# Kernel optimization log

Measured on AMD Instinct MI355X. Metric: run time of the kernel, lower is better.

The kernel has to match this reference:

```python
import jax, jax.numpy as jnp
import numpy as np

DENSITY = 985.0  # kg/m^3, body density used by BodyMeasurements for mass
EPS = 1e-12


def _measure(v_shaped, faces_tensor, circ_vert_idx, height_vert_idx):
    # Gather triangles: [B, F, 3(verts), 3(xyz)]
    tris = v_shaped[:, faces_tensor]
    v0, v1, v2 = tris[:, :, 0, :], tris[:, :, 1, :], tris[:, :, 2, :]

    # --- mass: signed tetrahedron volumes summed over faces ---
    vol = jnp.einsum('bfi,bfi->b', v0, jnp.cross(v1, v2)) / 6.0
    mass = jnp.abs(vol) * DENSITY                       # [B]

    # --- height: vertical distance between two landmark vertices ---
    height = jnp.abs(v_shaped[:, height_vert_idx[0], 1]
                     - v_shaped[:, height_vert_idx[1], 1])  # [B]

    # --- circumferences: horizontal plane y = y(landmark) intersected with mesh ---
    plane_y = v_shaped[:, circ_vert_idx, 1]             # [B, M] per-batch plane heights
    pa = tris                                           # edge starts  [B,F,3,3]
    pb = jnp.roll(tris, -1, axis=2)                     # edge ends    [B,F,3,3]
    ya = pa[..., 1]                                     # [B,F,3]
    yb = pb[..., 1]
    py = plane_y[:, None, None, :]                      # [B,1,1,M]
    da = ya[..., None] - py                             # signed dist of edge start [B,F,3,M]
    db = yb[..., None] - py
    crossing = (da * db) < 0.0                          # edge straddles plane
    t = da / jnp.where(crossing, da - db, 1.0)          # safe param along edge
    # intersection points on the plane: [B,F,3(edges),M,3]
    pts = pa[..., None, :] + t[..., None] * (pb - pa)[..., None, :]
    # a crossing triangle has exactly 2 crossing edges -> one active edge pair
    pts_n = jnp.roll(pts, -1, axis=2)
    pair_ok = crossing & jnp.roll(crossing, -1, axis=2)  # [B,F,3,M]
    d = jnp.where(pair_ok[..., None], pts_n - pts, 0.0)
    seg_len = jnp.sqrt(jnp.sum(d * d, axis=-1) + EPS) * pair_ok  # [B,F,3,M]
    circ = jnp.sum(seg_len, axis=(1, 2))                # [B, M]

    # mass, height, chest, waist, hips -> [B, 5]
    return jnp.concatenate([mass[:, None], height[:, None], circ], axis=1)


def setup_inputs() -> dict:
    key = jax.random.key(0)
    k1, k2, k3, k4 = jax.random.split(key, 4)
    B, V, F = 256, 6890, 13776
    v_shaped = jax.random.normal(k1, (B, V, 3), dtype=jnp.float32)
    faces_tensor = jax.random.randint(k2, (F, 3), 0, V)
    circ_vert_idx = jax.random.randint(k3, (3,), 0, V)
    height_vert_idx = jax.random.randint(k4, (2,), 0, V)
    return {
        'v_shaped': v_shaped,
        'faces_tensor': faces_tensor,
        'circ_vert_idx': circ_vert_idx,
        'height_vert_idx': height_vert_idx,
    }


def reference(v_shaped, faces_tensor, circ_vert_idx, height_vert_idx):
    return _measure(v_shaped, faces_tensor, circ_vert_idx, height_vert_idx)
```

## Files before the change

### kernel.cpp

```cpp
#include <hip/hip_runtime.h>
#include <math.h>

#define NV      6890
#define BLOCK   1024
#define NWAVES  (BLOCK / 64)
#define DENSITY 985.0f
#define EPS     1e-12f

typedef float v2f __attribute__((ext_vector_type(2)));

__device__ __forceinline__ float frcp(float x)  { return __builtin_amdgcn_rcpf(x); }
__device__ __forceinline__ float fsqrt(float x) { return __builtin_amdgcn_sqrtf(x); }

__global__ __launch_bounds__(BLOCK) void measure_kernel(
    const float* __restrict__ v,
    const int*   __restrict__ faces,
    const int*   __restrict__ circ_idx,
    const int*   __restrict__ h_idx,
    float*       __restrict__ out,
    int F)
{
    extern __shared__ float lds[];
    v2f*   xzs = reinterpret_cast<v2f*>(lds);
    float* ys  = lds + 2 * NV;
    float* red = ys + NV;

    const int b = blockIdx.x;
    const float* vb = v + (size_t)b * NV * 3;

    for (int i = threadIdx.x; i < NV; i += BLOCK) {
        const float* p = vb + 3 * i;
        const float x = p[0], y = p[1], z = p[2];
        ys[i] = y;
        xzs[i] = (v2f){ x, z };
    }
    __syncthreads();

    const float pys[3] = { ys[circ_idx[0]], ys[circ_idx[1]], ys[circ_idx[2]] };

    float vol = 0.0f;
    float circ[3] = {0.0f, 0.0f, 0.0f};

    #pragma unroll 2
    for (int f = threadIdx.x; f < F; f += BLOCK) {
        const int i0 = faces[3 * f + 0];
        const int i1 = faces[3 * f + 1];
        const int i2 = faces[3 * f + 2];

        const float y0 = ys[i0], y1 = ys[i1], y2 = ys[i2];
        const v2f xz0 = xzs[i0];
        const v2f xz1 = xzs[i1];
        const v2f xz2 = xzs[i2];

        {
            const float cx = y1 * xz2.y - xz1.y * y2;
            const float cy = xz1.y * xz2.x - xz1.x * xz2.y;
            const float cz = xz1.x * y2 - y1 * xz2.x;
            vol += xz0.x * cx + y0 * cy + xz0.y * cz;
        }

        const float r01 = frcp(y0 - y1);
        const float r12 = frcp(y1 - y2);
        const float r20 = frcp(y2 - y0);
        const v2f e01 = xz1 - xz0;
        const v2f e12 = xz2 - xz1;
        const v2f e20 = xz0 - xz2;

        #pragma unroll
        for (int p = 0; p < 3; ++p) {
            const float py = pys[p];
            const float d0 = y0 - py;
            const float d1 = y1 - py;
            const float d2 = y2 - py;
            const bool c0 = (d0 * d1) < 0.0f;
            const bool c1 = (d1 * d2) < 0.0f;
            const bool c2 = (d2 * d0) < 0.0f;

            const float t0 = d0 * r01;
            const float t1 = d1 * r12;
            const float t2 = d2 * r20;

            const v2f q0 = t0 * e01 + xz0;
            const v2f q1 = t1 * e12 + xz1;
            const v2f q2 = t2 * e20 + xz2;

            const v2f qA = c0 ? q0 : q1;
            const v2f qB = c2 ? q2 : q1;
            const bool any = c0 || c1 || c2;

            const v2f  d  = qA - qB;
            const float L = fsqrt(fmaf(d.x, d.x, fmaf(d.y, d.y, EPS)));
            circ[p] += any ? L : 0.0f;
        }
    }

    #pragma unroll
    for (int off = 32; off > 0; off >>= 1) {
        vol     += __shfl_down(vol,     off);
        circ[0] += __shfl_down(circ[0], off);
        circ[1] += __shfl_down(circ[1], off);
        circ[2] += __shfl_down(circ[2], off);
    }
    const int lane = threadIdx.x & 63;
    const int wid  = threadIdx.x >> 6;
    if (lane == 0) {
        red[wid * 4 + 0] = vol;
        red[wid * 4 + 1] = circ[0];
        red[wid * 4 + 2] = circ[1];
        red[wid * 4 + 3] = circ[2];
    }
    __syncthreads();

    if (threadIdx.x == 0) {
        float tv = 0.f, t0 = 0.f, t1 = 0.f, t2 = 0.f;
        for (int w = 0; w < NWAVES; ++w) {
            tv += red[w * 4 + 0];
            t0 += red[w * 4 + 1];
            t1 += red[w * 4 + 2];
            t2 += red[w * 4 + 3];
        }
        const float mass = fabsf(tv / 6.0f) * DENSITY;
        const float hy0 = ys[h_idx[0]];
        const float hy1 = ys[h_idx[1]];
        out[b * 5 + 0] = mass;
        out[b * 5 + 1] = fabsf(hy0 - hy1);
        out[b * 5 + 2] = t0;
        out[b * 5 + 3] = t1;
        out[b * 5 + 4] = t2;
    }
}

extern "C" void kernel_launch(void* const* d_in, const int* in_sizes, int n_in,
                              void* d_out, int out_size, void* d_ws, size_t ws_size,
                              hipStream_t stream) {
    const float* v        = (const float*)d_in[0];
    const int*   faces    = (const int*)d_in[1];
    const int*   circ_idx = (const int*)d_in[2];
    const int*   h_idx    = (const int*)d_in[3];
    float*       out      = (float*)d_out;

    const int B = in_sizes[0] / (NV * 3);
    const int F = in_sizes[1] / 3;

    const size_t lds_bytes = (size_t)(3 * NV + NWAVES * 4) * sizeof(float);
    measure_kernel<<<B, BLOCK, lds_bytes, stream>>>(v, faces, circ_idx, h_idx, out, F);
}
```

Before: 19.28 us.

## Factor plane-independent segment length per triangle and vectorize vertex staging loads

Rewrites each circumference segment length as |d_sel| times a per-triangle constant. The constant is the norm of the difference of edge gradients. Three square roots are now computed once per triangle instead of once per plane, which removes the per-plane intersection point arithmetic. Vertex staging into LDS now uses 8-byte loads over vertex pairs. This drops the EPS term inside the square root and changes the validity test to require two crossing edges, so results can differ slightly from the reference.

New measurement: 18.44 us. 4.3% less time.

```diff
diff --git a/kernel.cpp b/kernel.cpp
--- a/kernel.cpp
+++ b/kernel.cpp
@@ -5,7 +5,6 @@
 #define BLOCK   1024
 #define NWAVES  (BLOCK / 64)
 #define DENSITY 985.0f
-#define EPS     1e-12f
 
 typedef float v2f __attribute__((ext_vector_type(2)));
 
@@ -28,11 +27,18 @@
     const int b = blockIdx.x;
     const float* vb = v + (size_t)b * NV * 3;
 
-    for (int i = threadIdx.x; i < NV; i += BLOCK) {
-        const float* p = vb + 3 * i;
-        const float x = p[0], y = p[1], z = p[2];
-        ys[i] = y;
-        xzs[i] = (v2f){ x, z };
+    {
+        const v2f* vb2 = reinterpret_cast<const v2f*>(vb);
+        const int NSLOT = NV / 2;
+        for (int j = threadIdx.x; j < NSLOT; j += BLOCK) {
+            const v2f a = vb2[3 * j + 0];
+            const v2f m = vb2[3 * j + 1];
+            const v2f c = vb2[3 * j + 2];
+            ys[2 * j + 0] = a.y;
+            ys[2 * j + 1] = c.x;
+            xzs[2 * j + 0] = (v2f){ a.x, m.x };
+            xzs[2 * j + 1] = (v2f){ m.y, c.y };
+        }
     }
     __syncthreads();
 
@@ -59,12 +65,16 @@
             vol += xz0.x * cx + y0 * cy + xz0.y * cz;
         }
 
-        const float r01 = frcp(y0 - y1);
-        const float r12 = frcp(y1 - y2);
-        const float r20 = frcp(y2 - y0);
-        const v2f e01 = xz1 - xz0;
-        const v2f e12 = xz2 - xz1;
-        const v2f e20 = xz0 - xz2;
+        const v2f g01 = (xz1 - xz0) * frcp(y0 - y1);
+        const v2f g12 = (xz2 - xz1) * frcp(y1 - y2);
+        const v2f g20 = (xz0 - xz2) * frcp(y2 - y0);
+
+        const v2f w0 = g01 - g20;
+        const v2f w1 = g01 - g12;
+        const v2f w2 = g12 - g20;
+        const float h0 = fsqrt(fmaf(w0.x, w0.x, w0.y * w0.y));
+        const float h1 = fsqrt(fmaf(w1.x, w1.x, w1.y * w1.y));
+        const float h2 = fsqrt(fmaf(w2.x, w2.x, w2.y * w2.y));
 
         #pragma unroll
         for (int p = 0; p < 3; ++p) {
@@ -76,21 +86,14 @@
             const bool c1 = (d1 * d2) < 0.0f;
             const bool c2 = (d2 * d0) < 0.0f;
 
-            const float t0 = d0 * r01;
-            const float t1 = d1 * r12;
-            const float t2 = d2 * r20;
+            float dsel = c2 ? d0 : d1;
+            float hsel = c2 ? h0 : h1;
+            dsel = c0 ? dsel : d2;
+            hsel = c0 ? hsel : h2;
+            const bool valid = (c0 && c1) || (c1 && c2) || (c2 && c0);
 
-            const v2f q0 = t0 * e01 + xz0;
-            const v2f q1 = t1 * e12 + xz1;
-            const v2f q2 = t2 * e20 + xz2;
-
-            const v2f qA = c0 ? q0 : q1;
-            const v2f qB = c2 ? q2 : q1;
-            const bool any = c0 || c1 || c2;
-
-            const v2f  d  = qA - qB;
-            const float L = fsqrt(fmaf(d.x, d.x, fmaf(d.y, d.y, EPS)));
-            circ[p] += any ? L : 0.0f;
+            const float L = fabsf(dsel) * hsel;
+            circ[p] += valid ? L : 0.0f;
         }
     }
 
```
